# Performance work log

Hardware: AMD Instinct MI355X
Metric: run time of the kernel (lower is better)

## Reference

```python
import jax, jax.numpy as jnp
import numpy as np

DIM = 1024
N_HEADS = 16
HEAD_DIM = DIM // N_HEADS


def setup_inputs() -> dict:
    key = jax.random.key(0)
    ks = jax.random.split(key, 5)
    scale = 1.0 / np.sqrt(DIM)
    x = jax.random.normal(ks[0], (2, 2048, DIM), dtype=jnp.float32)
    W_qkv = jax.random.normal(ks[1], (DIM, 3 * DIM), dtype=jnp.float32) * scale
    b_qkv = jax.random.normal(ks[2], (3 * DIM,), dtype=jnp.float32) * 0.01
    W_proj = jax.random.normal(ks[3], (DIM, DIM), dtype=jnp.float32) * scale
    b_proj = jax.random.normal(ks[4], (DIM,), dtype=jnp.float32) * 0.01
    return {"x": x, "W_qkv": W_qkv, "b_qkv": b_qkv, "W_proj": W_proj, "b_proj": b_proj}


def reference(x, W_qkv, b_qkv, W_proj, b_proj):
    B, T, C = x.shape
    qkv = x @ W_qkv + b_qkv  # [B,T,3C]
    q, k, v = jnp.split(qkv, 3, axis=2)
    # [B,T,C] -> [B,H,T,Dh]
    def heads(y):
        return y.reshape(B, T, N_HEADS, HEAD_DIM).transpose(0, 2, 1, 3)
    q, k, v = heads(q), heads(k), heads(v)
    inv_sqrt_dh = 1.0 / jnp.sqrt(jnp.asarray(HEAD_DIM, dtype=x.dtype))
    attn = jnp.einsum('bhqd,bhkd->bhqk', q, k) * inv_sqrt_dh
    attn = jax.nn.softmax(attn, axis=-1)
    out = jnp.einsum('bhqk,bhkd->bhqd', attn, v)
    out = out.transpose(0, 2, 1, 3).reshape(B, T, C)
    return out @ W_proj + b_proj
```

## Files before the change

kernel.cpp:

```cpp
#include <hip/hip_runtime.h>
#include <hip/hip_bf16.h>
#include <math.h>

using bf16 = __hip_bfloat16;

typedef __bf16 bf16x8 __attribute__((ext_vector_type(8)));
typedef __bf16 bf16x4 __attribute__((ext_vector_type(4)));
typedef float  f32x4  __attribute__((ext_vector_type(4)));

constexpr int Bb = 2;
constexpr int Ts = 2048;
constexpr int Cc = 1024;
constexpr int Hh = 16;
constexpr int Dh = 64;
constexpr int Mm = Bb * Ts;
constexpr int Nqkv = 3 * Cc;
constexpr int BHTD = Bb * Hh * Ts * Dh;

__device__ __forceinline__
void gll16(const __bf16* g, __bf16* l)
{
    __builtin_amdgcn_global_load_lds(
        (const __attribute__((address_space(1))) unsigned int*)g,
        (__attribute__((address_space(3))) unsigned int*)l,
        16, 0, 0);
}

__global__ __launch_bounds__(256)
void cvt_bf16(const float* __restrict__ in, __bf16* __restrict__ out)
{
    int i = (blockIdx.x * 256 + threadIdx.x) * 4;
    float4 v = *(const float4*)(in + i);
    bf16x4 o = { (__bf16)v.x, (__bf16)v.y, (__bf16)v.z, (__bf16)v.w };
    *(bf16x4*)(out + i) = o;
}

__global__ __launch_bounds__(256)
void cvt_transpose(const float* __restrict__ W, __bf16* __restrict__ Wt, int cols)
{
    __shared__ __bf16 tl[64][72];
    const int t  = threadIdx.x;
    const int c0 = blockIdx.x * 64;
    const int r0 = blockIdx.y * 64;
    #pragma unroll
    for (int i = 0; i < 4; i++) {
        int e = t + 256 * i;
        int r = e >> 4, c4 = (e & 15) * 4;
        float4 v = *(const float4*)(W + (r0 + r) * cols + c0 + c4);
        bf16x4 o = { (__bf16)v.x, (__bf16)v.y, (__bf16)v.z, (__bf16)v.w };
        *(bf16x4*)&tl[r][c4] = o;
    }
    __syncthreads();
    #pragma unroll
    for (int i = 0; i < 4; i++) {
        int e = t + 256 * i;
        int n = e >> 4, k4 = (e & 15) * 4;
        bf16x4 o = { tl[k4][n], tl[k4 + 1][n], tl[k4 + 2][n], tl[k4 + 3][n] };
        *(bf16x4*)(Wt + (c0 + n) * 1024 + r0 + k4) = o;
    }
}

__device__ __forceinline__
void gemm_core(const __bf16* __restrict__ A, const __bf16* __restrict__ Bt,
               int m0, int n0, int wm, int wn, int quad, int l16, int t,
               f32x4 (&acc)[4][4])
{
    __shared__ __bf16 Al[128][32];
    __shared__ __bf16 Bl[128][32];

    const int wave = t >> 6;
    const int lane = t & 63;
    const int srow = lane >> 2;
    const int scol = (lane & 3) * 8;

    const __bf16* Ag = A  + (size_t)(m0 + wave * 16 + srow) * 1024 + scol;
    const __bf16* Bg = Bt + (size_t)(n0 + wave * 16 + srow) * 1024 + scol;
    __bf16* Al_lo = &Al[wave * 16][0];
    __bf16* Al_hi = &Al[64 + wave * 16][0];
    __bf16* Bl_lo = &Bl[wave * 16][0];
    __bf16* Bl_hi = &Bl[64 + wave * 16][0];

    for (int k0 = 0; k0 < 1024; k0 += 32) {
        gll16(Ag + k0,             Al_lo);
        gll16(Ag + k0 + 64 * 1024, Al_hi);
        gll16(Bg + k0,             Bl_lo);
        gll16(Bg + k0 + 64 * 1024, Bl_hi);
        __syncthreads();
        bf16x8 af[4], bfr[4];
        #pragma unroll
        for (int mt = 0; mt < 4; mt++)
            af[mt] = *(const bf16x8*)&Al[wm * 64 + mt * 16 + l16][quad * 8];
        #pragma unroll
        for (int nt = 0; nt < 4; nt++)
            bfr[nt] = *(const bf16x8*)&Bl[wn * 64 + nt * 16 + l16][quad * 8];
        #pragma unroll
        for (int mt = 0; mt < 4; mt++)
            #pragma unroll
            for (int nt = 0; nt < 4; nt++)
                acc[mt][nt] = __builtin_amdgcn_mfma_f32_16x16x32_bf16(
                    af[mt], bfr[nt], acc[mt][nt], 0, 0, 0);
        __syncthreads();
    }
}

__global__ __launch_bounds__(256)
void qkv_mfma(const __bf16* __restrict__ A, const __bf16* __restrict__ Bt,
              const float* __restrict__ bias, __bf16* __restrict__ qkv)
{
    const int t    = threadIdx.x;
    const int wave = t >> 6;
    const int lane = t & 63;
    const int quad = lane >> 4;
    const int l16  = lane & 15;
    const int wm   = wave >> 1, wn = wave & 1;
    const int n0 = blockIdx.x * 128;
    const int m0 = blockIdx.y * 128;

    f32x4 acc[4][4];
    #pragma unroll
    for (int i = 0; i < 4; i++)
        #pragma unroll
        for (int j = 0; j < 4; j++)
            acc[i][j] = f32x4{0.f, 0.f, 0.f, 0.f};

    gemm_core(A, Bt, m0, n0, wm, wn, quad, l16, t, acc);

    #pragma unroll
    for (int nt = 0; nt < 4; nt++) {
        int n = n0 + wn * 64 + nt * 16 + l16;
        float bs = bias[n];
        int which = n >> 10;
        int c = n & 1023;
        int h = c >> 6;
        int d = c & 63;
        if (which == 2) {
            #pragma unroll
            for (int mt = 0; mt < 4; mt++) {
                int m = m0 + wm * 64 + mt * 16 + quad * 4;
                int b = m >> 11;
                int tt = m & 2047;
                bf16x4 o = { (__bf16)(acc[mt][nt][0] + bs),
                             (__bf16)(acc[mt][nt][1] + bs),
                             (__bf16)(acc[mt][nt][2] + bs),
                             (__bf16)(acc[mt][nt][3] + bs) };
                *(bf16x4*)&qkv[2 * (size_t)BHTD +
                               (((size_t)(b * 16 + h) * 64 + d) * 2048 + tt)] = o;
            }
        } else {
            #pragma unroll
            for (int mt = 0; mt < 4; mt++) {
                #pragma unroll
                for (int r = 0; r < 4; r++) {
                    int m = m0 + wm * 64 + mt * 16 + quad * 4 + r;
                    int b = m >> 11;
                    int tt = m & 2047;
                    qkv[which * (size_t)BHTD +
                        (((b * 16 + h) * 2048 + tt) * 64 + d)] =
                        (__bf16)(acc[mt][nt][r] + bs);
                }
            }
        }
    }
}

__global__ __launch_bounds__(256)
void proj_mfma(const __bf16* __restrict__ A, const __bf16* __restrict__ Bt,
               const float* __restrict__ bias, float* __restrict__ out)
{
    const int t    = threadIdx.x;
    const int wave = t >> 6;
    const int lane = t & 63;
    const int quad = lane >> 4;
    const int l16  = lane & 15;
    const int wm   = wave >> 1, wn = wave & 1;
    const int n0 = blockIdx.x * 128;
    const int m0 = blockIdx.y * 128;

    f32x4 acc[4][4];
    #pragma unroll
    for (int i = 0; i < 4; i++)
        #pragma unroll
        for (int j = 0; j < 4; j++)
            acc[i][j] = f32x4{0.f, 0.f, 0.f, 0.f};

    gemm_core(A, Bt, m0, n0, wm, wn, quad, l16, t, acc);

    #pragma unroll
    for (int nt = 0; nt < 4; nt++) {
        int n = n0 + wn * 64 + nt * 16 + l16;
        float bs = bias[n];
        #pragma unroll
        for (int mt = 0; mt < 4; mt++) {
            #pragma unroll
            for (int r = 0; r < 4; r++) {
                int m = m0 + wm * 64 + mt * 16 + quad * 4 + r;
                out[m * 1024 + n] = acc[mt][nt][r] + bs;
            }
        }
    }
}

__global__ __launch_bounds__(256)
void attn_mfma(const __bf16* __restrict__ Q, const __bf16* __restrict__ K,
               const __bf16* __restrict__ VT, __bf16* __restrict__ O)
{
    __shared__ __bf16 Ks[64][72];
    __shared__ __bf16 Vt[64][72];
    __shared__ __bf16 Pl[4][16][72];

    const int t    = threadIdx.x;
    const int wave = t >> 6;
    const int lane = t & 63;
    const int quad = lane >> 4;
    const int l16  = lane & 15;

    const int bh = blockIdx.y;
    const int q0 = blockIdx.x * 64 + wave * 16;

    const __bf16* Qp = Q + (bh * Ts + q0) * Dh;
    const __bf16* Kp = K + (size_t)bh * Ts * Dh;
    const __bf16* Vp = VT + (size_t)bh * Dh * Ts;

    bf16x8 qf0 = *(const bf16x8*)(Qp + l16 * Dh + quad * 8);
    bf16x8 qf1 = *(const bf16x8*)(Qp + l16 * Dh + quad * 8 + 32);
    #pragma unroll
    for (int i = 0; i < 8; i++) {
        qf0[i] = (__bf16)(0.125f * (float)qf0[i]);
        qf1[i] = (__bf16)(0.125f * (float)qf1[i]);
    }

    const f32x4 zero4 = {0.f, 0.f, 0.f, 0.f};
    f32x4 accO[4];
    #pragma unroll
    for (int dt = 0; dt < 4; dt++) accO[dt] = zero4;
    float lsum = 0.f;

    const int jr = t >> 3;
    const int cc = (t & 7) * 8;
    const __bf16* Kb = Kp + jr * Dh + cc;
    const __bf16* Vb = Vp + jr * Ts + cc;

    uint4 ka0 = *(const uint4*)(Kb);
    uint4 ka1 = *(const uint4*)(Kb + 32 * Dh);
    uint4 va0 = *(const uint4*)(Vb);
    uint4 va1 = *(const uint4*)(Vb + 32 * Ts);

    for (int ic = 0; ic < Ts / 64; ic++) {
        *(uint4*)&Ks[jr][cc]      = ka0;
        *(uint4*)&Ks[jr + 32][cc] = ka1;
        *(uint4*)&Vt[jr][cc]      = va0;
        *(uint4*)&Vt[jr + 32][cc] = va1;
        if (ic < Ts / 64 - 1) {
            int ko = (ic + 1) * 64;
            ka0 = *(const uint4*)(Kb + ko * Dh);
            ka1 = *(const uint4*)(Kb + ko * Dh + 32 * Dh);
            va0 = *(const uint4*)(Vb + ko);
            va1 = *(const uint4*)(Vb + ko + 32 * Ts);
        }
        __syncthreads();

        f32x4 st[4];
        #pragma unroll
        for (int kt = 0; kt < 4; kt++) {
            bf16x8 k0f = *(const bf16x8*)(&Ks[kt * 16 + l16][quad * 8]);
            bf16x8 k1f = *(const bf16x8*)(&Ks[kt * 16 + l16][quad * 8 + 32]);
            f32x4 a = zero4;
            a = __builtin_amdgcn_mfma_f32_16x16x32_bf16(k0f, qf0, a, 0, 0, 0);
            a = __builtin_amdgcn_mfma_f32_16x16x32_bf16(k1f, qf1, a, 0, 0, 0);
            st[kt] = a;
        }

        #pragma unroll
        for (int kt = 0; kt < 4; kt++) {
            bf16x4 pb;
            #pragma unroll
            for (int r = 0; r < 4; r++) {
                float p = __expf(st[kt][r]);
                pb[r] = (__bf16)p;
                lsum += (float)pb[r];
            }
            *(bf16x4*)&Pl[wave][l16][kt * 16 + quad * 4] = pb;
        }
        bf16x8 pa0 = *(const bf16x8*)(&Pl[wave][l16][quad * 8]);
        bf16x8 pa1 = *(const bf16x8*)(&Pl[wave][l16][quad * 8 + 32]);

        #pragma unroll
        for (int dt = 0; dt < 4; dt++) {
            bf16x8 vb0 = *(const bf16x8*)(&Vt[l16 + 16 * dt][quad * 8]);
            bf16x8 vb1 = *(const bf16x8*)(&Vt[l16 + 16 * dt][quad * 8 + 32]);
            accO[dt] = __builtin_amdgcn_mfma_f32_16x16x32_bf16(pa0, vb0, accO[dt], 0, 0, 0);
            accO[dt] = __builtin_amdgcn_mfma_f32_16x16x32_bf16(pa1, vb1, accO[dt], 0, 0, 0);
        }
        __syncthreads();
    }

    lsum += __shfl_xor(lsum, 16);
    lsum += __shfl_xor(lsum, 32);

    int b = bh >> 4, h = bh & 15;
    __bf16* Op = O + ((long)(b * Ts + q0) * Cc) + h * 64;
    #pragma unroll
    for (int r = 0; r < 4; r++) {
        float inv = 1.f / __shfl(lsum, quad * 4 + r);
        int qrow = quad * 4 + r;
        #pragma unroll
        for (int dt = 0; dt < 4; dt++)
            Op[qrow * Cc + l16 + 16 * dt] = (__bf16)(accO[dt][r] * inv);
    }
}

extern "C" void kernel_launch(void* const* d_in, const int* in_sizes, int n_in,
                              void* d_out, int out_size, void* d_ws, size_t ws_size,
                              hipStream_t stream)
{
    (void)in_sizes; (void)n_in; (void)out_size; (void)ws_size;
    const float* x     = (const float*)d_in[0];
    const float* Wqkv  = (const float*)d_in[1];
    const float* bqkv  = (const float*)d_in[2];
    const float* Wproj = (const float*)d_in[3];
    const float* bproj = (const float*)d_in[4];
    float* out = (float*)d_out;

    __bf16* ws   = (__bf16*)d_ws;
    __bf16* Qw   = ws;
    __bf16* XbAO = ws + 3 * (size_t)BHTD;
    __bf16* Wqt  = XbAO + (size_t)Mm * Cc;
    __bf16* Wpt  = Wqt + (size_t)Nqkv * Cc;

    cvt_bf16<<<Mm * Cc / 1024, 256, 0, stream>>>(x, XbAO);
    cvt_transpose<<<dim3(Nqkv / 64, Cc / 64), 256, 0, stream>>>(Wqkv, Wqt, Nqkv);
    cvt_transpose<<<dim3(Cc / 64, Cc / 64), 256, 0, stream>>>(Wproj, Wpt, Cc);
    qkv_mfma<<<dim3(Nqkv / 128, Mm / 128), 256, 0, stream>>>(XbAO, Wqt, bqkv, Qw);
    attn_mfma<<<dim3(Ts / 64, Bb * Hh), 256, 0, stream>>>(
        Qw, Qw + BHTD, Qw + 2 * (size_t)BHTD, XbAO);
    proj_mfma<<<dim3(Cc / 128, Mm / 128), 256, 0, stream>>>(XbAO, Wpt, bproj, out);
}
```

Baseline: 212.4 us.

## Process 32 query rows per wave in attention to reuse K/V tiles

Each wave in the attention kernel now handles two 16-row query subtiles, so each block covers 128 queries. Every K and V fragment loaded from shared memory feeds twice as many MFMAs, and the grid is halved to 512 blocks. Block IDs are also remapped so that consecutive blocks land on different batch-head pairs, which may spread K/V reads across XCD caches. The cost is higher register use (two accumulator sets and two sets of scores) and fewer blocks to fill the GPU.

```diff
diff --git a/kernel.cpp b/kernel.cpp
--- a/kernel.cpp
+++ b/kernel.cpp
@@ -206,7 +206,7 @@
 {
     __shared__ __bf16 Ks[64][72];
     __shared__ __bf16 Vt[64][72];
-    __shared__ __bf16 Pl[4][16][72];
+    __shared__ __bf16 Pl[4][32][72];
 
     const int t    = threadIdx.x;
     const int wave = t >> 6;
@@ -214,98 +214,122 @@
     const int quad = lane >> 4;
     const int l16  = lane & 15;
 
-    const int bh = blockIdx.y;
-    const int q0 = blockIdx.x * 64 + wave * 16;
-
-    const __bf16* Qp = Q + (bh * Ts + q0) * Dh;
+    const int blk = blockIdx.x;
+    const int bh  = (blk & 7) * 4 + ((blk >> 3) & 3);
+    const int qc  = blk >> 5;
+    const int q0  = qc * 128 + wave * 32;
+
+    const __bf16* Qp = Q + ((size_t)bh * Ts + q0) * Dh;
     const __bf16* Kp = K + (size_t)bh * Ts * Dh;
     const __bf16* Vp = VT + (size_t)bh * Dh * Ts;
 
-    bf16x8 qf0 = *(const bf16x8*)(Qp + l16 * Dh + quad * 8);
-    bf16x8 qf1 = *(const bf16x8*)(Qp + l16 * Dh + quad * 8 + 32);
-    #pragma unroll
-    for (int i = 0; i < 8; i++) {
-        qf0[i] = (__bf16)(0.125f * (float)qf0[i]);
-        qf1[i] = (__bf16)(0.125f * (float)qf1[i]);
+    bf16x8 qf[2][2];
+    #pragma unroll
+    for (int s = 0; s < 2; s++) {
+        qf[s][0] = *(const bf16x8*)(Qp + (s * 16 + l16) * Dh + quad * 8);
+        qf[s][1] = *(const bf16x8*)(Qp + (s * 16 + l16) * Dh + quad * 8 + 32);
+        #pragma unroll
+        for (int i = 0; i < 8; i++) {
+            qf[s][0][i] = (__bf16)(0.125f * (float)qf[s][0][i]);
+            qf[s][1][i] = (__bf16)(0.125f * (float)qf[s][1][i]);
+        }
     }
 
     const f32x4 zero4 = {0.f, 0.f, 0.f, 0.f};
-    f32x4 accO[4];
-    #pragma unroll
-    for (int dt = 0; dt < 4; dt++) accO[dt] = zero4;
-    float lsum = 0.f;
+    f32x4 accO[2][4];
+    #pragma unroll
+    for (int s = 0; s < 2; s++)
+        #pragma unroll
+        for (int dt = 0; dt < 4; dt++) accO[s][dt] = zero4;
+    float lsum[2] = {0.f, 0.f};
 
     const int jr = t >> 3;
     const int cc = (t & 7) * 8;
     const __bf16* Kb = Kp + jr * Dh + cc;
     const __bf16* Vb = Vp + jr * Ts + cc;
 
-    uint4 ka0 = *(const uint4*)(Kb);
-    uint4 ka1 = *(const uint4*)(Kb + 32 * Dh);
-    uint4 va0 = *(const uint4*)(Vb);
-    uint4 va1 = *(const uint4*)(Vb + 32 * Ts);
+    bf16x8 ka0 = *(const bf16x8*)(Kb);
+    bf16x8 ka1 = *(const bf16x8*)(Kb + 32 * Dh);
+    bf16x8 va0 = *(const bf16x8*)(Vb);
+    bf16x8 va1 = *(const bf16x8*)(Vb + 32 * Ts);
 
     for (int ic = 0; ic < Ts / 64; ic++) {
-        *(uint4*)&Ks[jr][cc]      = ka0;
-        *(uint4*)&Ks[jr + 32][cc] = ka1;
-        *(uint4*)&Vt[jr][cc]      = va0;
-        *(uint4*)&Vt[jr + 32][cc] = va1;
+        *(bf16x8*)&Ks[jr][cc]      = ka0;
+        *(bf16x8*)&Ks[jr + 32][cc] = ka1;
+        *(bf16x8*)&Vt[jr][cc]      = va0;
+        *(bf16x8*)&Vt[jr + 32][cc] = va1;
         if (ic < Ts / 64 - 1) {
             int ko = (ic + 1) * 64;
-            ka0 = *(const uint4*)(Kb + ko * Dh);
-            ka1 = *(const uint4*)(Kb + ko * Dh + 32 * Dh);
-            va0 = *(const uint4*)(Vb + ko);
-            va1 = *(const uint4*)(Vb + ko + 32 * Ts);
+            ka0 = *(const bf16x8*)(Kb + ko * Dh);
+            ka1 = *(const bf16x8*)(Kb + ko * Dh + 32 * Dh);
+            va0 = *(const bf16x8*)(Vb + ko);
+            va1 = *(const bf16x8*)(Vb + ko + 32 * Ts);
         }
         __syncthreads();
 
-        f32x4 st[4];
+        f32x4 st[2][4];
         #pragma unroll
         for (int kt = 0; kt < 4; kt++) {
             bf16x8 k0f = *(const bf16x8*)(&Ks[kt * 16 + l16][quad * 8]);
             bf16x8 k1f = *(const bf16x8*)(&Ks[kt * 16 + l16][quad * 8 + 32]);
-            f32x4 a = zero4;
-            a = __builtin_amdgcn_mfma_f32_16x16x32_bf16(k0f, qf0, a, 0, 0, 0);
-            a = __builtin_amdgcn_mfma_f32_16x16x32_bf16(k1f, qf1, a, 0, 0, 0);
-            st[kt] = a;
-        }
-
-        #pragma unroll
-        for (int kt = 0; kt < 4; kt++) {
-            bf16x4 pb;
-            #pragma unroll
-            for (int r = 0; r < 4; r++) {
-                float p = __expf(st[kt][r]);
-                pb[r] = (__bf16)p;
-                lsum += (float)pb[r];
-            }
-            *(bf16x4*)&Pl[wave][l16][kt * 16 + quad * 4] = pb;
-        }
-        bf16x8 pa0 = *(const bf16x8*)(&Pl[wave][l16][quad * 8]);
-        bf16x8 pa1 = *(const bf16x8*)(&Pl[wave][l16][quad * 8 + 32]);
+            #pragma unroll
+            for (int s = 0; s < 2; s++) {
+                f32x4 a = zero4;
+                a = __builtin_amdgcn_mfma_f32_16x16x32_bf16(k0f, qf[s][0], a, 0, 0, 0);
+                a = __builtin_amdgcn_mfma_f32_16x16x32_bf16(k1f, qf[s][1], a, 0, 0, 0);
+                st[s][kt] = a;
+            }
+        }
+
+        #pragma unroll
+        for (int s = 0; s < 2; s++) {
+            #pragma unroll
+            for (int kt = 0; kt < 4; kt++) {
+                bf16x4 pb;
+                #pragma unroll
+                for (int r = 0; r < 4; r++) {
+                    float p = __expf(st[s][kt][r]);
+                    pb[r] = (__bf16)p;
+                    lsum[s] += (float)pb[r];
+                }
+                *(bf16x4*)&Pl[wave][s * 16 + l16][kt * 16 + quad * 4] = pb;
+            }
+        }
+        bf16x8 pa[2][2];
+        #pragma unroll
+        for (int s = 0; s < 2; s++) {
+            pa[s][0] = *(const bf16x8*)(&Pl[wave][s * 16 + l16][quad * 8]);
+            pa[s][1] = *(const bf16x8*)(&Pl[wave][s * 16 + l16][quad * 8 + 32]);
+        }
 
         #pragma unroll
         for (int dt = 0; dt < 4; dt++) {
             bf16x8 vb0 = *(const bf16x8*)(&Vt[l16 + 16 * dt][quad * 8]);
             bf16x8 vb1 = *(const bf16x8*)(&Vt[l16 + 16 * dt][quad * 8 + 32]);
-            accO[dt] = __builtin_amdgcn_mfma_f32_16x16x32_bf16(pa0, vb0, accO[dt], 0, 0, 0);
-            accO[dt] = __builtin_amdgcn_mfma_f32_16x16x32_bf16(pa1, vb1, accO[dt], 0, 0, 0);
+            #pragma unroll
+            for (int s = 0; s < 2; s++) {
+                accO[s][dt] = __builtin_amdgcn_mfma_f32_16x16x32_bf16(pa[s][0], vb0, accO[s][dt], 0, 0, 0);
+                accO[s][dt] = __builtin_amdgcn_mfma_f32_16x16x32_bf16(pa[s][1], vb1, accO[s][dt], 0, 0, 0);
+            }
         }
         __syncthreads();
     }
 
-    lsum += __shfl_xor(lsum, 16);
-    lsum += __shfl_xor(lsum, 32);
-
     int b = bh >> 4, h = bh & 15;
-    __bf16* Op = O + ((long)(b * Ts + q0) * Cc) + h * 64;
-    #pragma unroll
-    for (int r = 0; r < 4; r++) {
-        float inv = 1.f / __shfl(lsum, quad * 4 + r);
-        int qrow = quad * 4 + r;
-        #pragma unroll
-        for (int dt = 0; dt < 4; dt++)
-            Op[qrow * Cc + l16 + 16 * dt] = (__bf16)(accO[dt][r] * inv);
+    #pragma unroll
+    for (int s = 0; s < 2; s++) {
+        float l = lsum[s];
+        l += __shfl_xor(l, 16);
+        l += __shfl_xor(l, 32);
+        __bf16* Op = O + ((long)(b * Ts + q0 + s * 16) * Cc) + h * 64;
+        #pragma unroll
+        for (int r = 0; r < 4; r++) {
+            float inv = 1.f / __shfl(l, quad * 4 + r);
+            int qrow = quad * 4 + r;
+            #pragma unroll
+            for (int dt = 0; dt < 4; dt++)
+                Op[qrow * Cc + l16 + 16 * dt] = (__bf16)(accO[s][dt][r] * inv);
+        }
     }
 }
 
@@ -331,7 +355,7 @@
     cvt_transpose<<<dim3(Nqkv / 64, Cc / 64), 256, 0, stream>>>(Wqkv, Wqt, Nqkv);
     cvt_transpose<<<dim3(Cc / 64, Cc / 64), 256, 0, stream>>>(Wproj, Wpt, Cc);
     qkv_mfma<<<dim3(Nqkv / 128, Mm / 128), 256, 0, stream>>>(XbAO, Wqt, bqkv, Qw);
-    attn_mfma<<<dim3(Ts / 64, Bb * Hh), 256, 0, stream>>>(
+    attn_mfma<<<dim3(512), 256, 0, stream>>>(
         Qw, Qw + BHTD, Qw + 2 * (size_t)BHTD, XbAO);
     proj_mfma<<<dim3(Cc / 128, Mm / 128), 256, 0, stream>>>(XbAO, Wpt, bproj, out);
 }
```

Result: no change. 209.7 us (-1.3%).
